# Performance work log

Measured on AMD Instinct MI355X. Metric: run time of the kernel, lower is better.

## Reference

```python
import jax, jax.numpy as jnp
import numpy as np

C = 256
CQK = C // 8  # query/key projection dim (in_dim // 8)
B, H, W = 4, 64, 64


def setup_inputs() -> dict:
    key = jax.random.key(0)
    ks = jax.random.split(key, 7)
    scale = 0.05
    x = jax.random.normal(ks[0], (B, C, H, W), dtype=jnp.float32)
    Wq = jax.random.normal(ks[1], (CQK, C), dtype=jnp.float32) * scale
    bq = jax.random.normal(ks[2], (CQK,), dtype=jnp.float32) * scale
    Wk = jax.random.normal(ks[3], (CQK, C), dtype=jnp.float32) * scale
    bk = jax.random.normal(ks[4], (CQK,), dtype=jnp.float32) * scale
    Wv = jax.random.normal(ks[5], (C, C), dtype=jnp.float32) * scale
    bv = jax.random.normal(ks[6], (C,), dtype=jnp.float32) * scale
    return {"x": x, "Wq": Wq, "bq": bq, "Wk": Wk, "bk": bk, "Wv": Wv, "bv": bv}


def reference(x, Wq, bq, Wk, bk, Wv, bv):
    b, c, h, w = x.shape
    n = h * w
    xf = x.reshape(b, c, n)  # [B, C, N]
    # 1x1 convs == per-pixel linear maps over channels
    q = jnp.einsum('dc,bcn->bnd', Wq, xf) + bq[None, None, :]   # [B, N, C/8]
    k = jnp.einsum('dc,bcn->bdn', Wk, xf) + bk[None, :, None]   # [B, C/8, N]
    v = jnp.einsum('dc,bcn->bdn', Wv, xf) + bv[None, :, None]   # [B, C, N]
    energy = jnp.einsum('bnd,bdm->bnm', q, k)                    # [B, N, N]
    attention = jax.nn.softmax(energy, axis=-1)                  # softmax over keys
    # out = V @ attention^T  (torch: bmm(proj_value, attention.permute(0,2,1)))
    out = jnp.einsum('bdm,bnm->bdn', v, attention)               # [B, C, N]
    return out.reshape(b, c, h, w) + x
```

## Files before the change

### kernel.cpp

```cpp
#include <hip/hip_runtime.h>
#include <math.h>

#define BATCH 4
#define CH    256
#define NPIX  4096
#define DQK   32

typedef short          s16;
typedef unsigned int   uint_t;
typedef __attribute__((ext_vector_type(8))) short short8;
typedef __attribute__((ext_vector_type(4))) float floatx4;

__device__ __forceinline__ s16 f2bf(float f) {
  union { float f; uint_t u; } v; v.f = f;
  return (s16)((v.u + 0x8000u) >> 16);
}
__device__ __forceinline__ uint_t pk2(float a, float b) {
  union { float f; uint_t u; } x, y; x.f = a; y.f = b;
  return (((y.u + 0x8000u) >> 16) << 16) | ((x.u + 0x8000u) >> 16);
}

__global__ __launch_bounds__(256) void prepack(
    const float* __restrict__ Wq, const float* __restrict__ bq,
    const float* __restrict__ Wk, const float* __restrict__ bk,
    const float* __restrict__ Wv, const float* __restrict__ bv,
    s16* __restrict__ Wbf, float* __restrict__ Bsw)
{
  const int gid = blockIdx.x * 256 + threadIdx.x;
  const int e0  = gid * 4;
  const int row = e0 >> 8, col = e0 & 255;
  const float* src = (row < 32) ? Wq + (size_t)row * 256
                   : (row < 64) ? Wk + (size_t)(row - 32) * 256
                                : Wv + (size_t)(row - 64) * 256;
  float4 f = *(const float4*)(src + col);
  uint2 o; o.x = pk2(f.x, f.y); o.y = pk2(f.z, f.w);
  *(uint2*)(Wbf + e0) = o;
  if (gid < 320)
    Bsw[gid] = (gid < 32) ? bq[gid] : (gid < 64) ? bk[gid - 32] : bv[gid - 64];
}

__global__ __launch_bounds__(256, 2) void proj_mfma(
    const float* __restrict__ x, const s16* __restrict__ Wbf,
    const float* __restrict__ Bsw,
    s16* __restrict__ Qw, s16* __restrict__ Kw, s16* __restrict__ Vw)
{
  const int b  = blockIdx.x >> 7;
  const int n0 = (blockIdx.x & 127) << 5;
  const int t  = threadIdx.x;

  __shared__ s16 Xs[32][264];
  __shared__ s16 Os[256][40];

  const float* xb = x + (size_t)b * CH * NPIX + n0;
  #pragma unroll
  for (int i = 0; i < 2; ++i) {
    int task = i * 256 + t;
    int ncg  = task & 7;
    int kcg  = task >> 3;
    const float* src = xb + (size_t)(kcg * 4) * NPIX + ncg * 4;
    float rows[4][4];
    *(float4*)&rows[0][0] = *(const float4*)(src);
    *(float4*)&rows[1][0] = *(const float4*)(src + NPIX);
    *(float4*)&rows[2][0] = *(const float4*)(src + 2 * NPIX);
    *(float4*)&rows[3][0] = *(const float4*)(src + 3 * NPIX);
    #pragma unroll
    for (int c = 0; c < 4; ++c) {
      uint2 pk;
      pk.x = pk2(rows[0][c], rows[1][c]);
      pk.y = pk2(rows[2][c], rows[3][c]);
      *(uint2*)&Xs[ncg * 4 + c][kcg * 4] = pk;
    }
  }
  __syncthreads();

  const int w    = t >> 6;
  const int l15  = t & 15;
  const int quad = (t & 63) >> 4;

  floatx4 acc[5][2];
  #pragma unroll
  for (int si = 0; si < 5; ++si)
    #pragma unroll
    for (int nt = 0; nt < 2; ++nt) acc[si][nt] = (floatx4){0.f, 0.f, 0.f, 0.f};

  short8 afc[5], afn[5];
  #pragma unroll
  for (int si = 0; si < 5; ++si) {
    const int s = w + si * 4;
    afc[si] = *(const short8*)(Wbf + (size_t)(s * 16 + l15) * 256 + quad * 8);
  }
  for (int kc = 0; kc < 8; ++kc) {
    const int k0  = kc * 32;
    const int kn0 = (kc < 7) ? k0 + 32 : 0;
    #pragma unroll
    for (int si = 0; si < 5; ++si) {
      const int s = w + si * 4;
      afn[si] = *(const short8*)(Wbf + (size_t)(s * 16 + l15) * 256 + kn0 + quad * 8);
    }
    short8 bf[2];
    #pragma unroll
    for (int nt = 0; nt < 2; ++nt)
      bf[nt] = *(const short8*)&Xs[l15 + 16 * nt][k0 + quad * 8];
    #pragma unroll
    for (int si = 0; si < 5; ++si)
      #pragma unroll
      for (int nt = 0; nt < 2; ++nt)
        acc[si][nt] = __builtin_amdgcn_mfma_f32_16x16x32_bf16(afc[si], bf[nt], acc[si][nt], 0, 0, 0);
    #pragma unroll
    for (int si = 0; si < 5; ++si) afc[si] = afn[si];
  }

  #pragma unroll
  for (int si = 0; si < 5; ++si) {
    const int s = w + si * 4;
    float4 bb = *(const float4*)(Bsw + 16 * s + quad * 4);
    #pragma unroll
    for (int nt = 0; nt < 2; ++nt) {
      const int px  = 16 * nt + l15;
      float v0 = acc[si][nt][0] + bb.x;
      float v1 = acc[si][nt][1] + bb.y;
      float v2 = acc[si][nt][2] + bb.z;
      float v3 = acc[si][nt][3] + bb.w;
      if (s < 4) {
        s16* dst = (s < 2) ? Qw : Kw;
        int d0 = (s & 1) * 16 + quad * 4;
        uint2 pq; pq.x = pk2(v0, v1); pq.y = pk2(v2, v3);
        *(uint2*)(dst + ((size_t)b * NPIX + n0 + px) * DQK + d0) = pq;
      } else {
        const int c0 = (s - 4) * 16 + quad * 4;
        Os[c0 + 0][px] = f2bf(v0);
        Os[c0 + 1][px] = f2bf(v1);
        Os[c0 + 2][px] = f2bf(v2);
        Os[c0 + 3][px] = f2bf(v3);
      }
    }
  }
  __syncthreads();
  #pragma unroll
  for (int rep = 0; rep < 4; ++rep) {
    const int task = rep * 256 + t;
    const int ch   = task >> 2;
    const int seg  = task & 3;
    *(uint4*)(Vw + ((size_t)b * CH + ch) * NPIX + n0 + seg * 8) =
        *(const uint4*)&Os[ch][seg * 8];
  }
}

__global__ __launch_bounds__(512, 4) void attn_mfma(
    const s16* __restrict__ Qw, const s16* __restrict__ Kw,
    const s16* __restrict__ Vw, const float* __restrict__ x,
    float* __restrict__ out)
{
  const int bi = blockIdx.x;
  const int b  = (bi & 7) >> 1;
  const int h  = bi & 1;
  const int qt = bi >> 3;
  const int n0 = qt * 64;
  const int t  = threadIdx.x;
  const int w    = t >> 6;
  const int l15  = t & 15;
  const int quad = (t & 63) >> 4;
  const int cb   = h * 128 + 16 * w;

  __shared__ s16  Pt[2][64][136];
  __shared__ float Lsum[64][8];

  const s16* qbase = Qw + ((size_t)b * NPIX + n0) * DQK;
  short8 qb[4];
  #pragma unroll
  for (int tq = 0; tq < 4; ++tq)
    qb[tq] = *(const short8*)(qbase + (size_t)(16 * tq + l15) * DQK + quad * 8);

  floatx4 o[4];
  #pragma unroll
  for (int tq = 0; tq < 4; ++tq) o[tq] = (floatx4){0.f, 0.f, 0.f, 0.f};
  float l_part[4] = {0.f, 0.f, 0.f, 0.f};

  const s16* kbase = Kw + (size_t)b * NPIX * DQK;
  const s16* vbase = Vw + (size_t)b * CH * NPIX;

  short8 ka_c, ka_n, va[4];
  ka_c = *(const short8*)(kbase + (size_t)(16 * w + l15) * DQK + quad * 8);
  #pragma unroll
  for (int j = 0; j < 4; ++j)
    va[j] = *(const short8*)(vbase + (size_t)(cb + l15) * NPIX + 32 * j + quad * 8);

  int buf = 0;
  for (int kt = 0; kt < 32; ++kt) {
    const int m0  = kt * 128;
    const int mn0 = (kt < 31) ? m0 + 128 : 0;

    floatx4 sacc[4];
    #pragma unroll
    for (int tq = 0; tq < 4; ++tq)
      sacc[tq] = __builtin_amdgcn_mfma_f32_16x16x32_bf16(
                   ka_c, qb[tq], (floatx4){0.f, 0.f, 0.f, 0.f}, 0, 0, 0);

    ka_n = *(const short8*)(kbase + (size_t)(mn0 + 16 * w + l15) * DQK + quad * 8);

    #pragma unroll
    for (int tq = 0; tq < 4; ++tq) {
      float p0 = __expf(fminf(sacc[tq][0], 60.f));
      float p1 = __expf(fminf(sacc[tq][1], 60.f));
      float p2 = __expf(fminf(sacc[tq][2], 60.f));
      float p3 = __expf(fminf(sacc[tq][3], 60.f));
      l_part[tq] += (p0 + p1) + (p2 + p3);
      uint2 pk; pk.x = pk2(p0, p1); pk.y = pk2(p2, p3);
      *(uint2*)&Pt[buf][16 * tq + l15][16 * w + quad * 4] = pk;
    }
    __syncthreads();

    #pragma unroll
    for (int j = 0; j < 4; ++j) {
      short8 pb[4];
      #pragma unroll
      for (int tq = 0; tq < 4; ++tq)
        pb[tq] = *(const short8*)&Pt[buf][16 * tq + l15][32 * j + quad * 8];
      #pragma unroll
      for (int tq = 0; tq < 4; ++tq)
        o[tq] = __builtin_amdgcn_mfma_f32_16x16x32_bf16(va[j], pb[tq], o[tq], 0, 0, 0);
    }
    #pragma unroll
    for (int j = 0; j < 4; ++j)
      va[j] = *(const short8*)(vbase + (size_t)(cb + l15) * NPIX + mn0 + 32 * j + quad * 8);

    ka_c = ka_n;
    buf ^= 1;
  }

  #pragma unroll
  for (int tq = 0; tq < 4; ++tq) {
    l_part[tq] += __shfl_xor(l_part[tq], 16);
    l_part[tq] += __shfl_xor(l_part[tq], 32);
  }
  if (quad == 0) {
    #pragma unroll
    for (int tq = 0; tq < 4; ++tq) Lsum[16 * tq + l15][w] = l_part[tq];
  }
  __syncthreads();

  float inv[4];
  #pragma unroll
  for (int tq = 0; tq < 4; ++tq) {
    float4 s0 = *(const float4*)&Lsum[16 * tq + l15][0];
    float4 s1 = *(const float4*)&Lsum[16 * tq + l15][4];
    inv[tq] = 1.f / (((s0.x + s0.y) + (s0.z + s0.w)) + ((s1.x + s1.y) + (s1.z + s1.w)));
  }

  #pragma unroll
  for (int tq = 0; tq < 4; ++tq) {
    const int npx = n0 + 16 * tq + l15;
    #pragma unroll
    for (int r = 0; r < 4; ++r) {
      const int c = cb + quad * 4 + r;
      const size_t off = ((size_t)b * CH + c) * NPIX + npx;
      out[off] = fmaf(o[tq][r], inv[tq], x[off]);
    }
  }
}

extern "C" void kernel_launch(void* const* d_in, const int* in_sizes, int n_in,
                              void* d_out, int out_size, void* d_ws, size_t ws_size,
                              hipStream_t stream) {
  (void)in_sizes; (void)n_in; (void)out_size; (void)ws_size;
  const float* x  = (const float*)d_in[0];
  const float* Wq = (const float*)d_in[1];
  const float* bq = (const float*)d_in[2];
  const float* Wk = (const float*)d_in[3];
  const float* bk = (const float*)d_in[4];
  const float* Wv = (const float*)d_in[5];
  const float* bv = (const float*)d_in[6];
  float* out = (float*)d_out;

  unsigned char* ws = (unsigned char*)d_ws;
  s16*   Qw  = (s16*)ws;
  s16*   Kw  = (s16*)(ws + (size_t)1 * 1024 * 1024);
  s16*   Vw  = (s16*)(ws + (size_t)2 * 1024 * 1024);
  s16*   Wbf = (s16*)(ws + (size_t)10 * 1024 * 1024);
  float* Bsw = (float*)(ws + (size_t)10 * 1024 * 1024 + 256 * 1024);

  hipLaunchKernelGGL(prepack, dim3(80), dim3(256), 0, stream,
                     Wq, bq, Wk, bk, Wv, bv, Wbf, Bsw);
  hipLaunchKernelGGL(proj_mfma, dim3(512), dim3(256), 0, stream,
                     x, Wbf, Bsw, Qw, Kw, Vw);
  hipLaunchKernelGGL(attn_mfma, dim3(512), dim3(512), 0, stream,
                     Qw, Kw, Vw, x, out);
}
```

Before: 162.6 us.

## Warp-specialize attention into producer and consumer waves with LDS flag handshakes

```diff
diff --git a/kernel.cpp b/kernel.cpp
--- a/kernel.cpp
+++ b/kernel.cpp
@@ -158,104 +158,155 @@
   const int n0 = qt * 64;
   const int t  = threadIdx.x;
   const int w    = t >> 6;
+  const int ln   = t & 63;
   const int l15  = t & 15;
   const int quad = (t & 63) >> 4;
-  const int cb   = h * 128 + 16 * w;
 
   __shared__ s16  Pt[2][64][136];
-  __shared__ float Lsum[64][8];
-
-  const s16* qbase = Qw + ((size_t)b * NPIX + n0) * DQK;
-  short8 qb[4];
-  #pragma unroll
-  for (int tq = 0; tq < 4; ++tq)
-    qb[tq] = *(const short8*)(qbase + (size_t)(16 * tq + l15) * DQK + quad * 8);
-
-  floatx4 o[4];
-  #pragma unroll
-  for (int tq = 0; tq < 4; ++tq) o[tq] = (floatx4){0.f, 0.f, 0.f, 0.f};
-  float l_part[4] = {0.f, 0.f, 0.f, 0.f};
+  __shared__ __align__(16) float Lsum[64][4];
+  __shared__ int prod_done[2], cons_done[2];
+
+  if (t == 0) { prod_done[0] = 0; prod_done[1] = 0; cons_done[0] = 0; cons_done[1] = 0; }
+  __syncthreads();
 
   const s16* kbase = Kw + (size_t)b * NPIX * DQK;
   const s16* vbase = Vw + (size_t)b * CH * NPIX;
 
-  short8 ka_c, ka_n, va[4];
-  ka_c = *(const short8*)(kbase + (size_t)(16 * w + l15) * DQK + quad * 8);
-  #pragma unroll
-  for (int j = 0; j < 4; ++j)
-    va[j] = *(const short8*)(vbase + (size_t)(cb + l15) * NPIX + 32 * j + quad * 8);
-
-  int buf = 0;
-  for (int kt = 0; kt < 32; ++kt) {
-    const int m0  = kt * 128;
-    const int mn0 = (kt < 31) ? m0 + 128 : 0;
-
-    floatx4 sacc[4];
+  if (w < 4) {
+    const int p = w;
+    const s16* qbase = Qw + ((size_t)b * NPIX + n0) * DQK;
+    short8 qb[4];
     #pragma unroll
     for (int tq = 0; tq < 4; ++tq)
-      sacc[tq] = __builtin_amdgcn_mfma_f32_16x16x32_bf16(
-                   ka_c, qb[tq], (floatx4){0.f, 0.f, 0.f, 0.f}, 0, 0, 0);
-
-    ka_n = *(const short8*)(kbase + (size_t)(mn0 + 16 * w + l15) * DQK + quad * 8);
-
+      qb[tq] = *(const short8*)(qbase + (size_t)(16 * tq + l15) * DQK + quad * 8);
+
+    short8 ka_c[2], ka_n[2];
+    #pragma unroll
+    for (int sp = 0; sp < 2; ++sp)
+      ka_c[sp] = *(const short8*)(kbase + (size_t)(16 * (p + 4 * sp) + l15) * DQK + quad * 8);
+
+    float l_part[4] = {0.f, 0.f, 0.f, 0.f};
+
+    for (int kt = 0; kt < 32; ++kt) {
+      const int buf = kt & 1;
+      const int u   = kt >> 1;
+      const int mn0 = (kt < 31) ? (kt + 1) * 128 : 0;
+
+      floatx4 sacc[2][4];
+      #pragma unroll
+      for (int sp = 0; sp < 2; ++sp)
+        #pragma unroll
+        for (int tq = 0; tq < 4; ++tq)
+          sacc[sp][tq] = __builtin_amdgcn_mfma_f32_16x16x32_bf16(
+                           ka_c[sp], qb[tq], (floatx4){0.f, 0.f, 0.f, 0.f}, 0, 0, 0);
+      #pragma unroll
+      for (int sp = 0; sp < 2; ++sp)
+        ka_n[sp] = *(const short8*)(kbase + (size_t)(mn0 + 16 * (p + 4 * sp) + l15) * DQK + quad * 8);
+
+      const int tgt = 4 * u;
+      while (__hip_atomic_load(&cons_done[buf], __ATOMIC_ACQUIRE,
+                               __HIP_MEMORY_SCOPE_WORKGROUP) < tgt)
+        __builtin_amdgcn_s_sleep(1);
+
+      float ts[4] = {0.f, 0.f, 0.f, 0.f};
+      #pragma unroll
+      for (int sp = 0; sp < 2; ++sp) {
+        const int col = 16 * (p + 4 * sp) + quad * 4;
+        #pragma unroll
+        for (int tq = 0; tq < 4; ++tq) {
+          float p0 = __expf(sacc[sp][tq][0]);
+          float p1 = __expf(sacc[sp][tq][1]);
+          float p2 = __expf(sacc[sp][tq][2]);
+          float p3 = __expf(sacc[sp][tq][3]);
+          ts[tq] += (p0 + p1) + (p2 + p3);
+          uint2 pk; pk.x = pk2(p0, p1); pk.y = pk2(p2, p3);
+          *(uint2*)&Pt[buf][16 * tq + l15][col] = pk;
+        }
+      }
+      #pragma unroll
+      for (int tq = 0; tq < 4; ++tq) {
+        ts[tq] += __shfl_xor(ts[tq], 16);
+        ts[tq] += __shfl_xor(ts[tq], 32);
+        l_part[tq] += ts[tq];
+      }
+      if (ln == 0)
+        __hip_atomic_fetch_add(&prod_done[buf], 1, __ATOMIC_RELEASE,
+                               __HIP_MEMORY_SCOPE_WORKGROUP);
+      #pragma unroll
+      for (int sp = 0; sp < 2; ++sp) ka_c[sp] = ka_n[sp];
+    }
+    if (quad == 0) {
+      #pragma unroll
+      for (int tq = 0; tq < 4; ++tq) Lsum[16 * tq + l15][p] = l_part[tq];
+    }
+    __syncthreads();
+  } else {
+    const int c  = w - 4;
+    const int cb = h * 128 + 32 * c;
+
+    floatx4 o[2][4];
+    #pragma unroll
+    for (int cs = 0; cs < 2; ++cs)
+      #pragma unroll
+      for (int tq = 0; tq < 4; ++tq) o[cs][tq] = (floatx4){0.f, 0.f, 0.f, 0.f};
+
+    short8 va[2][4];
+    #pragma unroll
+    for (int cs = 0; cs < 2; ++cs)
+      #pragma unroll
+      for (int j = 0; j < 4; ++j)
+        va[cs][j] = *(const short8*)(vbase + (size_t)(cb + 16 * cs + l15) * NPIX
+                                     + 32 * j + quad * 8);
+
+    for (int kt = 0; kt < 32; ++kt) {
+      const int buf = kt & 1;
+      const int u   = kt >> 1;
+      const int mn0 = (kt < 31) ? (kt + 1) * 128 : 0;
+
+      const int tgt = 4 * (u + 1);
+      while (__hip_atomic_load(&prod_done[buf], __ATOMIC_ACQUIRE,
+                               __HIP_MEMORY_SCOPE_WORKGROUP) < tgt)
+        __builtin_amdgcn_s_sleep(1);
+
+      #pragma unroll
+      for (int j = 0; j < 4; ++j) {
+        short8 pb[4];
+        #pragma unroll
+        for (int tq = 0; tq < 4; ++tq)
+          pb[tq] = *(const short8*)&Pt[buf][16 * tq + l15][32 * j + quad * 8];
+        #pragma unroll
+        for (int cs = 0; cs < 2; ++cs) {
+          #pragma unroll
+          for (int tq = 0; tq < 4; ++tq)
+            o[cs][tq] = __builtin_amdgcn_mfma_f32_16x16x32_bf16(va[cs][j], pb[tq], o[cs][tq], 0, 0, 0);
+          va[cs][j] = *(const short8*)(vbase + (size_t)(cb + 16 * cs + l15) * NPIX
+                                       + mn0 + 32 * j + quad * 8);
+        }
+      }
+      if (ln == 0)
+        __hip_atomic_fetch_add(&cons_done[buf], 1, __ATOMIC_RELEASE,
+                               __HIP_MEMORY_SCOPE_WORKGROUP);
+    }
+    __syncthreads();
+
+    float inv[4];
     #pragma unroll
     for (int tq = 0; tq < 4; ++tq) {
-      float p0 = __expf(fminf(sacc[tq][0], 60.f));
-      float p1 = __expf(fminf(sacc[tq][1], 60.f));
-      float p2 = __expf(fminf(sacc[tq][2], 60.f));
-      float p3 = __expf(fminf(sacc[tq][3], 60.f));
-      l_part[tq] += (p0 + p1) + (p2 + p3);
-      uint2 pk; pk.x = pk2(p0, p1); pk.y = pk2(p2, p3);
-      *(uint2*)&Pt[buf][16 * tq + l15][16 * w + quad * 4] = pk;
-    }
-    __syncthreads();
-
-    #pragma unroll
-    for (int j = 0; j < 4; ++j) {
-      short8 pb[4];
-      #pragma unroll
-      for (int tq = 0; tq < 4; ++tq)
-        pb[tq] = *(const short8*)&Pt[buf][16 * tq + l15][32 * j + quad * 8];
-      #pragma unroll
-      for (int tq = 0; tq < 4; ++tq)
-        o[tq] = __builtin_amdgcn_mfma_f32_16x16x32_bf16(va[j], pb[tq], o[tq], 0, 0, 0);
-    }
-    #pragma unroll
-    for (int j = 0; j < 4; ++j)
-      va[j] = *(const short8*)(vbase + (size_t)(cb + l15) * NPIX + mn0 + 32 * j + quad * 8);
-
-    ka_c = ka_n;
-    buf ^= 1;
-  }
-
-  #pragma unroll
-  for (int tq = 0; tq < 4; ++tq) {
-    l_part[tq] += __shfl_xor(l_part[tq], 16);
-    l_part[tq] += __shfl_xor(l_part[tq], 32);
-  }
-  if (quad == 0) {
-    #pragma unroll
-    for (int tq = 0; tq < 4; ++tq) Lsum[16 * tq + l15][w] = l_part[tq];
-  }
-  __syncthreads();
-
-  float inv[4];
-  #pragma unroll
-  for (int tq = 0; tq < 4; ++tq) {
-    float4 s0 = *(const float4*)&Lsum[16 * tq + l15][0];
-    float4 s1 = *(const float4*)&Lsum[16 * tq + l15][4];
-    inv[tq] = 1.f / (((s0.x + s0.y) + (s0.z + s0.w)) + ((s1.x + s1.y) + (s1.z + s1.w)));
-  }
-
-  #pragma unroll
-  for (int tq = 0; tq < 4; ++tq) {
-    const int npx = n0 + 16 * tq + l15;
-    #pragma unroll
-    for (int r = 0; r < 4; ++r) {
-      const int c = cb + quad * 4 + r;
-      const size_t off = ((size_t)b * CH + c) * NPIX + npx;
-      out[off] = fmaf(o[tq][r], inv[tq], x[off]);
-    }
+      float4 s0 = *(const float4*)&Lsum[16 * tq + l15][0];
+      inv[tq] = 1.f / ((s0.x + s0.y) + (s0.z + s0.w));
+    }
+    #pragma unroll
+    for (int cs = 0; cs < 2; ++cs)
+      #pragma unroll
+      for (int tq = 0; tq < 4; ++tq) {
+        const int npx = n0 + 16 * tq + l15;
+        #pragma unroll
+        for (int r = 0; r < 4; ++r) {
+          const int ch = cb + 16 * cs + quad * 4 + r;
+          const size_t off = ((size_t)b * CH + ch) * NPIX + npx;
+          out[off] = fmaf(o[cs][tq][r], inv[tq], x[off]);
+        }
+      }
   }
 }
 
```

Measured after the change: 162.9 us. Within noise of the previous version (+0.2%).

## Split attention over key halves with full-channel blocks and 32x32 MFMA, add merge kernel

Applied to the files above, without the earlier changes.

```diff
diff --git a/kernel.cpp b/kernel.cpp
--- a/kernel.cpp
+++ b/kernel.cpp
@@ -8,12 +8,16 @@
 
 typedef short          s16;
 typedef unsigned int   uint_t;
-typedef __attribute__((ext_vector_type(8))) short short8;
-typedef __attribute__((ext_vector_type(4))) float floatx4;
+typedef __attribute__((ext_vector_type(8)))  short short8;
+typedef __attribute__((ext_vector_type(4)))  float floatx4;
+typedef __attribute__((ext_vector_type(16))) float floatx16;
 
 __device__ __forceinline__ s16 f2bf(float f) {
   union { float f; uint_t u; } v; v.f = f;
   return (s16)((v.u + 0x8000u) >> 16);
+}
+__device__ __forceinline__ float bf2f(s16 u) {
+  union { uint_t u; float f; } v; v.u = ((uint_t)(unsigned short)u) << 16; return v.f;
 }
 __device__ __forceinline__ uint_t pk2(float a, float b) {
   union { float f; uint_t u; } x, y; x.f = a; y.f = b;
@@ -148,19 +152,20 @@
 
 __global__ __launch_bounds__(512, 4) void attn_mfma(
     const s16* __restrict__ Qw, const s16* __restrict__ Kw,
-    const s16* __restrict__ Vw, const float* __restrict__ x,
-    float* __restrict__ out)
+    const s16* __restrict__ Vw, s16* __restrict__ Op, float* __restrict__ Lp)
 {
   const int bi = blockIdx.x;
   const int b  = (bi & 7) >> 1;
-  const int h  = bi & 1;
-  const int qt = bi >> 3;
+  const int ks = (bi >> 3) & 1;
+  const int qt = ((bi >> 4) << 1) | (bi & 1);
   const int n0 = qt * 64;
+  const int km0 = ks * 2048;
   const int t  = threadIdx.x;
   const int w    = t >> 6;
   const int l15  = t & 15;
   const int quad = (t & 63) >> 4;
-  const int cb   = h * 128 + 16 * w;
+  const int l31  = t & 31;
+  const int half = (t & 63) >> 5;
 
   __shared__ s16  Pt[2][64][136];
   __shared__ float Lsum[64][8];
@@ -171,24 +176,24 @@
   for (int tq = 0; tq < 4; ++tq)
     qb[tq] = *(const short8*)(qbase + (size_t)(16 * tq + l15) * DQK + quad * 8);
 
-  floatx4 o[4];
-  #pragma unroll
-  for (int tq = 0; tq < 4; ++tq) o[tq] = (floatx4){0.f, 0.f, 0.f, 0.f};
+  floatx16 o0, o1;
+  #pragma unroll
+  for (int i = 0; i < 16; ++i) { o0[i] = 0.f; o1[i] = 0.f; }
   float l_part[4] = {0.f, 0.f, 0.f, 0.f};
 
-  const s16* kbase = Kw + (size_t)b * NPIX * DQK;
-  const s16* vbase = Vw + (size_t)b * CH * NPIX;
-
-  short8 ka_c, ka_n, va[4];
-  ka_c = *(const short8*)(kbase + (size_t)(16 * w + l15) * DQK + quad * 8);
-  #pragma unroll
-  for (int j = 0; j < 4; ++j)
-    va[j] = *(const short8*)(vbase + (size_t)(cb + l15) * NPIX + 32 * j + quad * 8);
+  const s16* kbase = Kw + ((size_t)b * NPIX + km0) * DQK;
+  const s16* vrow  = Vw + ((size_t)b * CH + 32 * w + l31) * NPIX + km0;
+
+  short8 ka_c = *(const short8*)(kbase + (size_t)(16 * w + l15) * DQK + quad * 8);
+  short8 va[8];
+  #pragma unroll
+  for (int s = 0; s < 8; ++s)
+    va[s] = *(const short8*)(vrow + s * 16 + half * 8);
 
   int buf = 0;
-  for (int kt = 0; kt < 32; ++kt) {
+  for (int kt = 0; kt < 16; ++kt) {
     const int m0  = kt * 128;
-    const int mn0 = (kt < 31) ? m0 + 128 : 0;
+    const int mn0 = (kt < 15) ? m0 + 128 : 0;
 
     floatx4 sacc[4];
     #pragma unroll
@@ -196,67 +201,89 @@
       sacc[tq] = __builtin_amdgcn_mfma_f32_16x16x32_bf16(
                    ka_c, qb[tq], (floatx4){0.f, 0.f, 0.f, 0.f}, 0, 0, 0);
 
-    ka_n = *(const short8*)(kbase + (size_t)(mn0 + 16 * w + l15) * DQK + quad * 8);
+    short8 ka_n = *(const short8*)(kbase + (size_t)(mn0 + 16 * w + l15) * DQK + quad * 8);
 
     #pragma unroll
     for (int tq = 0; tq < 4; ++tq) {
-      float p0 = __expf(fminf(sacc[tq][0], 60.f));
-      float p1 = __expf(fminf(sacc[tq][1], 60.f));
-      float p2 = __expf(fminf(sacc[tq][2], 60.f));
-      float p3 = __expf(fminf(sacc[tq][3], 60.f));
-      l_part[tq] += (p0 + p1) + (p2 + p3);
+      float p0 = __expf(sacc[tq][0]);
+      float p1 = __expf(sacc[tq][1]);
+      float p2 = __expf(sacc[tq][2]);
+      float p3 = __expf(sacc[tq][3]);
+      float ts = (p0 + p1) + (p2 + p3);
       uint2 pk; pk.x = pk2(p0, p1); pk.y = pk2(p2, p3);
       *(uint2*)&Pt[buf][16 * tq + l15][16 * w + quad * 4] = pk;
+      ts += __shfl_xor(ts, 16);
+      ts += __shfl_xor(ts, 32);
+      l_part[tq] += ts;
     }
     __syncthreads();
 
     #pragma unroll
-    for (int j = 0; j < 4; ++j) {
-      short8 pb[4];
-      #pragma unroll
-      for (int tq = 0; tq < 4; ++tq)
-        pb[tq] = *(const short8*)&Pt[buf][16 * tq + l15][32 * j + quad * 8];
-      #pragma unroll
-      for (int tq = 0; tq < 4; ++tq)
-        o[tq] = __builtin_amdgcn_mfma_f32_16x16x32_bf16(va[j], pb[tq], o[tq], 0, 0, 0);
-    }
-    #pragma unroll
-    for (int j = 0; j < 4; ++j)
-      va[j] = *(const short8*)(vbase + (size_t)(cb + l15) * NPIX + mn0 + 32 * j + quad * 8);
-
+    for (int s = 0; s < 8; ++s) {
+      short8 pb0 = *(const short8*)&Pt[buf][l31][16 * s + half * 8];
+      short8 pb1 = *(const short8*)&Pt[buf][32 + l31][16 * s + half * 8];
+      o0 = __builtin_amdgcn_mfma_f32_32x32x16_bf16(va[s], pb0, o0, 0, 0, 0);
+      o1 = __builtin_amdgcn_mfma_f32_32x32x16_bf16(va[s], pb1, o1, 0, 0, 0);
+      va[s] = *(const short8*)(vrow + mn0 + 16 * s + half * 8);
+    }
     ka_c = ka_n;
     buf ^= 1;
   }
 
-  #pragma unroll
-  for (int tq = 0; tq < 4; ++tq) {
-    l_part[tq] += __shfl_xor(l_part[tq], 16);
-    l_part[tq] += __shfl_xor(l_part[tq], 32);
-  }
   if (quad == 0) {
     #pragma unroll
     for (int tq = 0; tq < 4; ++tq) Lsum[16 * tq + l15][w] = l_part[tq];
   }
   __syncthreads();
-
-  float inv[4];
-  #pragma unroll
-  for (int tq = 0; tq < 4; ++tq) {
-    float4 s0 = *(const float4*)&Lsum[16 * tq + l15][0];
-    float4 s1 = *(const float4*)&Lsum[16 * tq + l15][4];
-    inv[tq] = 1.f / (((s0.x + s0.y) + (s0.z + s0.w)) + ((s1.x + s1.y) + (s1.z + s1.w)));
-  }
-
-  #pragma unroll
-  for (int tq = 0; tq < 4; ++tq) {
-    const int npx = n0 + 16 * tq + l15;
-    #pragma unroll
-    for (int r = 0; r < 4; ++r) {
-      const int c = cb + quad * 4 + r;
-      const size_t off = ((size_t)b * CH + c) * NPIX + npx;
-      out[off] = fmaf(o[tq][r], inv[tq], x[off]);
-    }
-  }
+  if (t < 64) {
+    float4 s0 = *(const float4*)&Lsum[t][0];
+    float4 s1 = *(const float4*)&Lsum[t][4];
+    Lp[(((size_t)b * 2 + ks) * 64 + qt) * 64 + t] =
+        ((s0.x + s0.y) + (s0.z + s0.w)) + ((s1.x + s1.y) + (s1.z + s1.w));
+  }
+
+  s16* ob = Op + (((size_t)b * 2 + ks) * 64 + qt) * (256 * 64);
+  #pragma unroll
+  for (int reg = 0; reg < 16; ++reg) {
+    const int ch = 32 * w + (reg & 3) + 8 * (reg >> 2) + 4 * half;
+    ob[ch * 64 + l31]      = f2bf(o0[reg]);
+    ob[ch * 64 + 32 + l31] = f2bf(o1[reg]);
+  }
+}
+
+__global__ __launch_bounds__(256) void reduce_merge(
+    const s16* __restrict__ Op, const float* __restrict__ Lp,
+    const float* __restrict__ x, float* __restrict__ out)
+{
+  const size_t e0 = ((size_t)blockIdx.x * 256 + threadIdx.x) * 8;
+  const int n  = (int)(e0 & 4095);
+  const int ch = (int)((e0 >> 12) & 255);
+  const int b  = (int)(e0 >> 20);
+  const int qt = n >> 6, q = n & 63;
+
+  const size_t p0 = (((size_t)b * 2 + 0) * 64 + qt) * (256 * 64) + ch * 64 + q;
+  const size_t p1 = (((size_t)b * 2 + 1) * 64 + qt) * (256 * 64) + ch * 64 + q;
+  union { uint4 v; s16 u[8]; } O0, O1;
+  O0.v = *(const uint4*)(Op + p0);
+  O1.v = *(const uint4*)(Op + p1);
+
+  const float* l0p = Lp + (((size_t)b * 2 + 0) * 64 + qt) * 64 + q;
+  const float* l1p = Lp + (((size_t)b * 2 + 1) * 64 + qt) * 64 + q;
+  float4 l0a = *(const float4*)l0p, l0b = *(const float4*)(l0p + 4);
+  float4 l1a = *(const float4*)l1p, l1b = *(const float4*)(l1p + 4);
+  float linv[8] = {
+    1.f / (l0a.x + l1a.x), 1.f / (l0a.y + l1a.y),
+    1.f / (l0a.z + l1a.z), 1.f / (l0a.w + l1a.w),
+    1.f / (l0b.x + l1b.x), 1.f / (l0b.y + l1b.y),
+    1.f / (l0b.z + l1b.z), 1.f / (l0b.w + l1b.w) };
+
+  float4 xa = *(const float4*)(x + e0), xb = *(const float4*)(x + e0 + 4);
+  float r[8] = { xa.x, xa.y, xa.z, xa.w, xb.x, xb.y, xb.z, xb.w };
+  #pragma unroll
+  for (int j = 0; j < 8; ++j)
+    r[j] = fmaf(bf2f(O0.u[j]) + bf2f(O1.u[j]), linv[j], r[j]);
+  *(float4*)(out + e0)     = make_float4(r[0], r[1], r[2], r[3]);
+  *(float4*)(out + e0 + 4) = make_float4(r[4], r[5], r[6], r[7]);
 }
 
 extern "C" void kernel_launch(void* const* d_in, const int* in_sizes, int n_in,
@@ -278,11 +305,15 @@
   s16*   Vw  = (s16*)(ws + (size_t)2 * 1024 * 1024);
   s16*   Wbf = (s16*)(ws + (size_t)10 * 1024 * 1024);
   float* Bsw = (float*)(ws + (size_t)10 * 1024 * 1024 + 256 * 1024);
+  float* Lp  = (float*)(ws + (size_t)10 * 1024 * 1024 + 512 * 1024);
+  s16*   Op  = (s16*)(ws + (size_t)11 * 1024 * 1024);
 
   hipLaunchKernelGGL(prepack, dim3(80), dim3(256), 0, stream,
                      Wq, bq, Wk, bk, Wv, bv, Wbf, Bsw);
   hipLaunchKernelGGL(proj_mfma, dim3(512), dim3(256), 0, stream,
                      x, Wbf, Bsw, Qw, Kw, Vw);
   hipLaunchKernelGGL(attn_mfma, dim3(512), dim3(512), 0, stream,
-                     Qw, Kw, Vw, x, out);
-}
+                     Qw, Kw, Vw, Op, Lp);
+  hipLaunchKernelGGL(reduce_merge, dim3(2048), dim3(256), 0, stream,
+                     Op, Lp, x, out);
+}
```

After: 165.1 us. No clear change (+1.5%).
